# Kernel tuning notes

Hardware: AMD Instinct MI355X
Metric: run time of the kernel (lower is better)

## Reference

```python
import jax, jax.numpy as jnp
import numpy as np


def setup_inputs() -> dict:
    key = jax.random.key(0)
    k1, k2, k3 = jax.random.split(key, 3)
    B, C, H, W = 64, 512, 28, 28
    K = 32
    std = 1.0 / (K * C) ** 0.5
    x = jax.random.normal(k1, (B, C, H, W), dtype=jnp.float32)
    codewords = jax.random.uniform(k2, (K, C), dtype=jnp.float32, minval=-std, maxval=std)
    scale = jax.random.uniform(k3, (K,), dtype=jnp.float32, minval=-1.0, maxval=0.0)
    return {"x": x, "codewords": codewords, "scale": scale}


def reference(x, codewords, scale):
    # x: (B, C, H, W) -> descriptors (B, N, C)
    B, C, H, W = x.shape
    K = codewords.shape[0]
    xd = x.reshape(B, C, H * W).transpose(0, 2, 1)  # (B, N, C)

    # scaled L2: scale_k * ||x_n - c_k||^2, expanded without (B,N,K,C) intermediate
    x_sq = jnp.sum(xd * xd, axis=-1, keepdims=True)            # (B, N, 1)
    c_sq = jnp.sum(codewords * codewords, axis=-1)             # (K,)
    xc = jnp.einsum("bnc,kc->bnk", xd, codewords)              # (B, N, K)
    dist = scale * (x_sq - 2.0 * xc + c_sq)                    # (B, N, K)

    A = jax.nn.softmax(dist, axis=2)                           # (B, N, K)

    # encoded_k = sum_n A[b,n,k] * (x[b,n] - c[k])
    wx = jnp.einsum("bnk,bnc->bkc", A, xd)                     # (B, K, C)
    wsum = jnp.sum(A, axis=1)                                  # (B, K)
    encoded = wx - wsum[:, :, None] * codewords[None, :, :]    # (B, K, C)
    return encoded
```

## Files before the change

### kernel.cpp

```cpp
#include <hip/hip_runtime.h>
#include <hip/hip_bf16.h>

#define BB 64
#define CC 512
#define NPIX 784
#define KK 32
#define NSPL 13
#define PXB 64
#define CW_S 520
#define XS2_S 72

typedef __attribute__((ext_vector_type(8))) short short8;
typedef __attribute__((ext_vector_type(4))) float floatx4;
typedef __attribute__((ext_vector_type(4))) unsigned short ushort4v;

#define OFF_WP 0
#define OFF_WS (NSPL*BB*KK*CC)

__device__ __forceinline__ unsigned short f2bf(float f) {
    union { float f; unsigned u; } v; v.f = f;
    return (unsigned short)((v.u + 0x7FFFu + ((v.u >> 16) & 1u)) >> 16);
}
__device__ __forceinline__ float bf2f(unsigned short h) {
    union { unsigned u; float f; } v; v.u = ((unsigned)h) << 16; return v.f;
}

__global__ __launch_bounds__(256) void k_fused(const float* __restrict__ x,
                                               const float* __restrict__ cw,
                                               const float* __restrict__ scale,
                                               float* __restrict__ ws)
{
    __shared__ __align__(16) unsigned char u8[KK * CW_S * 2];
    __shared__ __align__(16) unsigned short A_l[KK * XS2_S];
    __shared__ float csq_p[8][KK];
    __shared__ float csq_l[KK];
    __shared__ float wred[KK][8];

    unsigned short* cs = (unsigned short*)u8;
    unsigned short* xs = (unsigned short*)u8;

    const int t     = threadIdx.x;
    const int lane  = t & 63;
    const int w     = t >> 6;
    const int col   = lane & 15;
    const int quad  = lane >> 4;
    const int split = blockIdx.x;
    const int b     = blockIdx.y;
    const int p0    = split * PXB;

#pragma unroll 4
    for (int j = 0; j < 16; ++j) {
        const int qidx = t + j * 256;
        const int row = qidx >> 7, qc = qidx & 127;
        const float4 v = *(const float4*)&cw[row * CC + qc * 4];
        ushort4v p; p.x = f2bf(v.x); p.y = f2bf(v.y); p.z = f2bf(v.z); p.w = f2bf(v.w);
        *(ushort4v*)&cs[row * CW_S + qc * 4] = p;
    }
    __syncthreads();
    {
        const int k = t & 31, part = t >> 5;
        float s = 0.f;
        for (int i = 0; i < 64; ++i) {
            const float v = bf2f(cs[k * CW_S + part * 64 + i]);
            s += v * v;
        }
        csq_p[part][k] = s;
    }
    __syncthreads();
    if (t < KK) {
        float s = 0.f;
#pragma unroll
        for (int p = 0; p < 8; ++p) s += csq_p[p][t];
        csq_l[t] = s;
    }
    __syncthreads();

    const float s0 = scale[col], s1 = scale[col + 16];
    const float q0 = csq_l[col], q1 = csq_l[col + 16];

    {
        const int pxg = p0 + w * 16 + col;
        const int px = (pxg < NPIX) ? pxg : (NPIX - 1);
        const float* xb = x + (size_t)b * CC * NPIX + px;

        floatx4 acc0 = {0.f, 0.f, 0.f, 0.f};
        floatx4 acc1 = {0.f, 0.f, 0.f, 0.f};
        float xsqp = 0.f;
        float va[8], vb[8];

#pragma unroll
        for (int j = 0; j < 8; ++j) va[j] = xb[(size_t)(quad * 8 + j) * NPIX];

#pragma unroll
        for (int kc = 0; kc < 16; kc += 2) {
            {
                const int cb = (kc + 1) * 32 + quad * 8;
#pragma unroll
                for (int j = 0; j < 8; ++j) vb[j] = xb[(size_t)(cb + j) * NPIX];
            }
            {
#pragma unroll
                for (int j = 0; j < 8; ++j) xsqp += va[j] * va[j];
                short8 a;
#pragma unroll
                for (int j = 0; j < 8; ++j) a[j] = (short)f2bf(va[j]);
                const int cb0 = kc * 32 + quad * 8;
                const short8 b0 = *(const short8*)&cs[col * CW_S + cb0];
                const short8 b1 = *(const short8*)&cs[(col + 16) * CW_S + cb0];
                acc0 = __builtin_amdgcn_mfma_f32_16x16x32_bf16(a, b0, acc0, 0, 0, 0);
                acc1 = __builtin_amdgcn_mfma_f32_16x16x32_bf16(a, b1, acc1, 0, 0, 0);
            }
            if (kc + 2 < 16) {
                const int cb = (kc + 2) * 32 + quad * 8;
#pragma unroll
                for (int j = 0; j < 8; ++j) va[j] = xb[(size_t)(cb + j) * NPIX];
            }
            {
#pragma unroll
                for (int j = 0; j < 8; ++j) xsqp += vb[j] * vb[j];
                short8 a;
#pragma unroll
                for (int j = 0; j < 8; ++j) a[j] = (short)f2bf(vb[j]);
                const int cb1 = (kc + 1) * 32 + quad * 8;
                const short8 b0 = *(const short8*)&cs[col * CW_S + cb1];
                const short8 b1 = *(const short8*)&cs[(col + 16) * CW_S + cb1];
                acc0 = __builtin_amdgcn_mfma_f32_16x16x32_bf16(a, b0, acc0, 0, 0, 0);
                acc1 = __builtin_amdgcn_mfma_f32_16x16x32_bf16(a, b1, acc1, 0, 0, 0);
            }
        }

        xsqp += __shfl_xor(xsqp, 16);
        xsqp += __shfl_xor(xsqp, 32);

#pragma unroll
        for (int r = 0; r < 4; ++r) {
            const int pl = w * 16 + quad * 4 + r;
            const float xq = __shfl(xsqp, quad * 4 + r);
            const float d0 = s0 * (xq + q0 - 2.f * acc0[r]);
            const float d1 = s1 * (xq + q1 - 2.f * acc1[r]);
            float mx = fmaxf(d0, d1);
            mx = fmaxf(mx, __shfl_xor(mx, 1));
            mx = fmaxf(mx, __shfl_xor(mx, 2));
            mx = fmaxf(mx, __shfl_xor(mx, 4));
            mx = fmaxf(mx, __shfl_xor(mx, 8));
            const float e0 = __expf(d0 - mx), e1 = __expf(d1 - mx);
            float sm = e0 + e1;
            sm += __shfl_xor(sm, 1);
            sm += __shfl_xor(sm, 2);
            sm += __shfl_xor(sm, 4);
            sm += __shfl_xor(sm, 8);
            const float inv = 1.f / sm;
            const bool valid = (p0 + pl) < NPIX;
            A_l[col * XS2_S + pl]        = valid ? f2bf(e0 * inv) : (unsigned short)0;
            A_l[(col + 16) * XS2_S + pl] = valid ? f2bf(e1 * inv) : (unsigned short)0;
        }
    }
    __syncthreads();

    {
        const int k = t >> 3, part = t & 7;
        float s = 0.f;
#pragma unroll
        for (int i = 0; i < 8; ++i) s += bf2f(A_l[k * XS2_S + part * 8 + i]);
        wred[k][part] = s;
    }
    __syncthreads();
    if (t < KK) {
        float s = 0.f;
#pragma unroll
        for (int p = 0; p < 8; ++p) s += wred[t][p];
        ws[OFF_WS + (size_t)(split * BB + b) * KK + t] = s;
    }

    const float* xbase = x + (size_t)b * CC * NPIX + p0;
    float* Wp = ws + OFF_WP;

    for (int cch = 0; cch < 4; ++cch) {
        __syncthreads();
#pragma unroll 2
        for (int j = 0; j < 8; ++j) {
            const int q = t + j * 256;
            const int row = q >> 4, pq = q & 15;
            ushort4v p;
            if (p0 + pq * 4 < NPIX) {
                const float4 v = *(const float4*)&xbase[(size_t)(cch * 128 + row) * NPIX + pq * 4];
                p.x = f2bf(v.x); p.y = f2bf(v.y); p.z = f2bf(v.z); p.w = f2bf(v.w);
            } else { p.x = 0; p.y = 0; p.z = 0; p.w = 0; }
            *(ushort4v*)&xs[row * XS2_S + pq * 4] = p;
        }
        __syncthreads();

        floatx4 a00 = {0.f,0.f,0.f,0.f}, a01 = {0.f,0.f,0.f,0.f};
        floatx4 a10 = {0.f,0.f,0.f,0.f}, a11 = {0.f,0.f,0.f,0.f};
#pragma unroll
        for (int ks = 0; ks < 2; ++ks) {
            const int off = ks * 32 + quad * 8;
            const short8 av0 = *(const short8*)&A_l[col * XS2_S + off];
            const short8 av1 = *(const short8*)&A_l[(col + 16) * XS2_S + off];
            const short8 bv0 = *(const short8*)&xs[(w * 32 + col) * XS2_S + off];
            const short8 bv1 = *(const short8*)&xs[(w * 32 + 16 + col) * XS2_S + off];
            a00 = __builtin_amdgcn_mfma_f32_16x16x32_bf16(av0, bv0, a00, 0, 0, 0);
            a10 = __builtin_amdgcn_mfma_f32_16x16x32_bf16(av1, bv0, a10, 0, 0, 0);
            a01 = __builtin_amdgcn_mfma_f32_16x16x32_bf16(av0, bv1, a01, 0, 0, 0);
            a11 = __builtin_amdgcn_mfma_f32_16x16x32_bf16(av1, bv1, a11, 0, 0, 0);
        }

        const size_t sb = (size_t)(split * BB + b) * KK;
        const int cb = cch * 128 + w * 32;
#pragma unroll
        for (int r = 0; r < 4; ++r) {
            const int k0 = quad * 4 + r;
            Wp[(sb + k0) * CC + cb + col]           = a00[r];
            Wp[(sb + k0) * CC + cb + 16 + col]      = a01[r];
            Wp[(sb + k0 + 16) * CC + cb + col]      = a10[r];
            Wp[(sb + k0 + 16) * CC + cb + 16 + col] = a11[r];
        }
    }
}

__global__ __launch_bounds__(256) void k3(const float* __restrict__ cw,
                                          const float* __restrict__ ws,
                                          float* __restrict__ out)
{
    const int idx = blockIdx.x * 256 + threadIdx.x;
    const int c4 = idx & 127;
    const int k  = (idx >> 7) & 31;
    const int b  = idx >> 12;

    const float* Wp = ws + OFF_WP;
    float4 s = make_float4(0.f, 0.f, 0.f, 0.f);
#pragma unroll
    for (int sp = 0; sp < NSPL; ++sp) {
        const float4 v = *(const float4*)&Wp[((size_t)(sp * BB + b) * KK + k) * CC + c4 * 4];
        s.x += v.x; s.y += v.y; s.z += v.z; s.w += v.w;
    }
    float wsum = 0.f;
#pragma unroll
    for (int sp = 0; sp < NSPL; ++sp) wsum += ws[OFF_WS + (size_t)(sp * BB + b) * KK + k];

    const float4 c4f = *(const float4*)&cw[k * CC + c4 * 4];
    float4 o;
    o.x = s.x - wsum * c4f.x;
    o.y = s.y - wsum * c4f.y;
    o.z = s.z - wsum * c4f.z;
    o.w = s.w - wsum * c4f.w;
    *(float4*)&out[(size_t)idx * 4] = o;
}

extern "C" void kernel_launch(void* const* d_in, const int* in_sizes, int n_in,
                              void* d_out, int out_size, void* d_ws, size_t ws_size,
                              hipStream_t stream) {
    const float* x     = (const float*)d_in[0];
    const float* cw    = (const float*)d_in[1];
    const float* scale = (const float*)d_in[2];
    float* out = (float*)d_out;
    float* ws  = (float*)d_ws;

    k_fused<<<dim3(NSPL, BB), dim3(256), 0, stream>>>(x, cw, scale, ws);
    k3<<<dim3(BB * KK * CC / 4 / 256), dim3(256), 0, stream>>>(cw, ws, out);
}
```

Measured before the change: 192.3 us.

## Precompute bf16 codeword fragments in prep kernel and stage x via async LDS loads

Adds a small prep kernel that converts the codewords once into MFMA-fragment-ordered bf16 and computes the codeword squared norms. Each fused block no longer rebuilds the converted codewords and their norms in shared memory, and reads B fragments directly from global or L2. The first GEMM stage now streams x into double-buffered LDS with global_load_lds, replacing strided per-thread global loads with coalesced 16-byte rows. The cost is an extra kernel launch, B fragments fetched from L2 rather than LDS, and a shared-memory layout that the later stage reuses. Codeword norms are now taken from the fp32 values rather than the bf16-rounded ones, which changes numerics slightly.

```diff
diff --git a/kernel.cpp b/kernel.cpp
--- a/kernel.cpp
+++ b/kernel.cpp
@@ -7,15 +7,17 @@
 #define KK 32
 #define NSPL 13
 #define PXB 64
-#define CW_S 520
+#define NCHK 8
 #define XS2_S 72
 
 typedef __attribute__((ext_vector_type(8))) short short8;
 typedef __attribute__((ext_vector_type(4))) float floatx4;
 typedef __attribute__((ext_vector_type(4))) unsigned short ushort4v;
 
-#define OFF_WP 0
-#define OFF_WS (NSPL*BB*KK*CC)
+#define OFF_BF  0
+#define OFF_CSQ 8192
+#define OFF_WP  8256
+#define OFF_WS2 (OFF_WP + NSPL*BB*KK*CC)
 
 __device__ __forceinline__ unsigned short f2bf(float f) {
     union { float f; unsigned u; } v; v.f = f;
@@ -25,19 +27,51 @@
     union { unsigned u; float f; } v; v.u = ((unsigned)h) << 16; return v.f;
 }
 
+__global__ __launch_bounds__(256) void kprep(const float* __restrict__ cw,
+                                             float* __restrict__ ws)
+{
+    const int t = threadIdx.x;
+    if (blockIdx.x < 8) {
+        const int idx  = blockIdx.x * 256 + t;
+        const int lane = idx & 63;
+        const int pair = idx >> 6;
+        const int row  = (pair & 1) * 16 + (lane & 15);
+        const int cb   = (pair >> 1) * 32 + (lane >> 4) * 8;
+        unsigned short* Bf = (unsigned short*)(ws + OFF_BF);
+        ushort4v pa, pb;
+        pa.x = f2bf(cw[row * CC + cb + 0]); pa.y = f2bf(cw[row * CC + cb + 1]);
+        pa.z = f2bf(cw[row * CC + cb + 2]); pa.w = f2bf(cw[row * CC + cb + 3]);
+        pb.x = f2bf(cw[row * CC + cb + 4]); pb.y = f2bf(cw[row * CC + cb + 5]);
+        pb.z = f2bf(cw[row * CC + cb + 6]); pb.w = f2bf(cw[row * CC + cb + 7]);
+        *(ushort4v*)&Bf[(size_t)idx * 8]     = pa;
+        *(ushort4v*)&Bf[(size_t)idx * 8 + 4] = pb;
+    } else {
+        __shared__ float red[8][KK];
+        const int k = t & 31, part = t >> 5;
+        float s = 0.f;
+#pragma unroll 4
+        for (int i = 0; i < 64; ++i) {
+            const float v = cw[k * CC + part * 64 + i];
+            s += v * v;
+        }
+        red[part][k] = s;
+        __syncthreads();
+        if (t < KK) {
+            float s2 = 0.f;
+#pragma unroll
+            for (int p = 0; p < 8; ++p) s2 += red[p][t];
+            ws[OFF_CSQ + t] = s2;
+        }
+    }
+}
+
 __global__ __launch_bounds__(256) void k_fused(const float* __restrict__ x,
-                                               const float* __restrict__ cw,
                                                const float* __restrict__ scale,
                                                float* __restrict__ ws)
 {
-    __shared__ __align__(16) unsigned char u8[KK * CW_S * 2];
+    __shared__ __align__(16) float xbuf[2][64 * 64];
     __shared__ __align__(16) unsigned short A_l[KK * XS2_S];
-    __shared__ float csq_p[8][KK];
-    __shared__ float csq_l[KK];
     __shared__ float wred[KK][8];
-
-    unsigned short* cs = (unsigned short*)u8;
-    unsigned short* xs = (unsigned short*)u8;
 
     const int t     = threadIdx.x;
     const int lane  = t & 63;
@@ -48,130 +82,96 @@
     const int b     = blockIdx.y;
     const int p0    = split * PXB;
 
-#pragma unroll 4
-    for (int j = 0; j < 16; ++j) {
-        const int qidx = t + j * 256;
-        const int row = qidx >> 7, qc = qidx & 127;
-        const float4 v = *(const float4*)&cw[row * CC + qc * 4];
-        ushort4v p; p.x = f2bf(v.x); p.y = f2bf(v.y); p.z = f2bf(v.z); p.w = f2bf(v.w);
-        *(ushort4v*)&cs[row * CW_S + qc * 4] = p;
+    const unsigned short* Bf = (const unsigned short*)(ws + OFF_BF);
+    const float* xlim = x + (size_t)BB * CC * NPIX - 4;
+
+    auto stage = [&](int ch, int buf) {
+#pragma unroll
+        for (int i = 0; i < 4; ++i) {
+            const int r0 = w * 16 + i * 4;
+            const float* g = x + ((size_t)b * CC + ch * 64 + r0 + (lane >> 4)) * NPIX
+                               + p0 + (lane & 15) * 4;
+            if (g > xlim) g = xlim;
+            __builtin_amdgcn_global_load_lds(
+                (const __attribute__((address_space(1))) void*)g,
+                (__attribute__((address_space(3))) void*)&xbuf[buf][r0 * 64],
+                16, 0, 0);
+        }
+    };
+
+    floatx4 acc0 = {0.f, 0.f, 0.f, 0.f};
+    floatx4 acc1 = {0.f, 0.f, 0.f, 0.f};
+    float xsqp = 0.f;
+
+    stage(0, 0);
+    for (int ch = 0; ch < NCHK; ++ch) {
+        __syncthreads();
+        if (ch + 1 < NCHK) stage(ch + 1, (ch + 1) & 1);
+        const float* xb = xbuf[ch & 1];
+#pragma unroll
+        for (int ks = 0; ks < 2; ++ks) {
+            const int kc = ch * 2 + ks;
+            float v[8];
+#pragma unroll
+            for (int j = 0; j < 8; ++j)
+                v[j] = xb[(ks * 32 + quad * 8 + j) * 64 + w * 16 + col];
+#pragma unroll
+            for (int j = 0; j < 8; ++j) xsqp += v[j] * v[j];
+            short8 a;
+#pragma unroll
+            for (int j = 0; j < 8; ++j) a[j] = (short)f2bf(v[j]);
+            const short8 b0 = *(const short8*)&Bf[(size_t)((kc * 2 + 0) * 64 + lane) * 8];
+            const short8 b1 = *(const short8*)&Bf[(size_t)((kc * 2 + 1) * 64 + lane) * 8];
+            acc0 = __builtin_amdgcn_mfma_f32_16x16x32_bf16(a, b0, acc0, 0, 0, 0);
+            acc1 = __builtin_amdgcn_mfma_f32_16x16x32_bf16(a, b1, acc1, 0, 0, 0);
+        }
+    }
+
+    xsqp += __shfl_xor(xsqp, 16);
+    xsqp += __shfl_xor(xsqp, 32);
+
+    const float s0 = scale[col], s1 = scale[col + 16];
+    const float q0 = ws[OFF_CSQ + col], q1 = ws[OFF_CSQ + col + 16];
+#pragma unroll
+    for (int r = 0; r < 4; ++r) {
+        const int pl = w * 16 + quad * 4 + r;
+        const float xq = __shfl(xsqp, quad * 4 + r);
+        const float d0 = s0 * (xq + q0 - 2.f * acc0[r]);
+        const float d1 = s1 * (xq + q1 - 2.f * acc1[r]);
+        float mx = fmaxf(d0, d1);
+        mx = fmaxf(mx, __shfl_xor(mx, 1));
+        mx = fmaxf(mx, __shfl_xor(mx, 2));
+        mx = fmaxf(mx, __shfl_xor(mx, 4));
+        mx = fmaxf(mx, __shfl_xor(mx, 8));
+        const float e0 = __expf(d0 - mx), e1 = __expf(d1 - mx);
+        float sm = e0 + e1;
+        sm += __shfl_xor(sm, 1);
+        sm += __shfl_xor(sm, 2);
+        sm += __shfl_xor(sm, 4);
+        sm += __shfl_xor(sm, 8);
+        const float inv = 1.f / sm;
+        const bool valid = (p0 + pl) < NPIX;
+        A_l[col * XS2_S + pl]        = valid ? f2bf(e0 * inv) : (unsigned short)0;
+        A_l[(col + 16) * XS2_S + pl] = valid ? f2bf(e1 * inv) : (unsigned short)0;
     }
     __syncthreads();
+
     {
-        const int k = t & 31, part = t >> 5;
+        const int k = t >> 3, part = t & 7;
         float s = 0.f;
-        for (int i = 0; i < 64; ++i) {
-            const float v = bf2f(cs[k * CW_S + part * 64 + i]);
-            s += v * v;
-        }
-        csq_p[part][k] = s;
+#pragma unroll
+        for (int i = 0; i < 8; ++i) s += bf2f(A_l[k * XS2_S + part * 8 + i]);
+        wred[k][part] = s;
     }
     __syncthreads();
     if (t < KK) {
         float s = 0.f;
 #pragma unroll
-        for (int p = 0; p < 8; ++p) s += csq_p[p][t];
-        csq_l[t] = s;
-    }
-    __syncthreads();
-
-    const float s0 = scale[col], s1 = scale[col + 16];
-    const float q0 = csq_l[col], q1 = csq_l[col + 16];
-
-    {
-        const int pxg = p0 + w * 16 + col;
-        const int px = (pxg < NPIX) ? pxg : (NPIX - 1);
-        const float* xb = x + (size_t)b * CC * NPIX + px;
-
-        floatx4 acc0 = {0.f, 0.f, 0.f, 0.f};
-        floatx4 acc1 = {0.f, 0.f, 0.f, 0.f};
-        float xsqp = 0.f;
-        float va[8], vb[8];
-
-#pragma unroll
-        for (int j = 0; j < 8; ++j) va[j] = xb[(size_t)(quad * 8 + j) * NPIX];
-
-#pragma unroll
-        for (int kc = 0; kc < 16; kc += 2) {
-            {
-                const int cb = (kc + 1) * 32 + quad * 8;
-#pragma unroll
-                for (int j = 0; j < 8; ++j) vb[j] = xb[(size_t)(cb + j) * NPIX];
-            }
-            {
-#pragma unroll
-                for (int j = 0; j < 8; ++j) xsqp += va[j] * va[j];
-                short8 a;
-#pragma unroll
-                for (int j = 0; j < 8; ++j) a[j] = (short)f2bf(va[j]);
-                const int cb0 = kc * 32 + quad * 8;
-                const short8 b0 = *(const short8*)&cs[col * CW_S + cb0];
-                const short8 b1 = *(const short8*)&cs[(col + 16) * CW_S + cb0];
-                acc0 = __builtin_amdgcn_mfma_f32_16x16x32_bf16(a, b0, acc0, 0, 0, 0);
-                acc1 = __builtin_amdgcn_mfma_f32_16x16x32_bf16(a, b1, acc1, 0, 0, 0);
-            }
-            if (kc + 2 < 16) {
-                const int cb = (kc + 2) * 32 + quad * 8;
-#pragma unroll
-                for (int j = 0; j < 8; ++j) va[j] = xb[(size_t)(cb + j) * NPIX];
-            }
-            {
-#pragma unroll
-                for (int j = 0; j < 8; ++j) xsqp += vb[j] * vb[j];
-                short8 a;
-#pragma unroll
-                for (int j = 0; j < 8; ++j) a[j] = (short)f2bf(vb[j]);
-                const int cb1 = (kc + 1) * 32 + quad * 8;
-                const short8 b0 = *(const short8*)&cs[col * CW_S + cb1];
-                const short8 b1 = *(const short8*)&cs[(col + 16) * CW_S + cb1];
-                acc0 = __builtin_amdgcn_mfma_f32_16x16x32_bf16(a, b0, acc0, 0, 0, 0);
-                acc1 = __builtin_amdgcn_mfma_f32_16x16x32_bf16(a, b1, acc1, 0, 0, 0);
-            }
-        }
-
-        xsqp += __shfl_xor(xsqp, 16);
-        xsqp += __shfl_xor(xsqp, 32);
-
-#pragma unroll
-        for (int r = 0; r < 4; ++r) {
-            const int pl = w * 16 + quad * 4 + r;
-            const float xq = __shfl(xsqp, quad * 4 + r);
-            const float d0 = s0 * (xq + q0 - 2.f * acc0[r]);
-            const float d1 = s1 * (xq + q1 - 2.f * acc1[r]);
-            float mx = fmaxf(d0, d1);
-            mx = fmaxf(mx, __shfl_xor(mx, 1));
-            mx = fmaxf(mx, __shfl_xor(mx, 2));
-            mx = fmaxf(mx, __shfl_xor(mx, 4));
-            mx = fmaxf(mx, __shfl_xor(mx, 8));
-            const float e0 = __expf(d0 - mx), e1 = __expf(d1 - mx);
-            float sm = e0 + e1;
-            sm += __shfl_xor(sm, 1);
-            sm += __shfl_xor(sm, 2);
-            sm += __shfl_xor(sm, 4);
-            sm += __shfl_xor(sm, 8);
-            const float inv = 1.f / sm;
-            const bool valid = (p0 + pl) < NPIX;
-            A_l[col * XS2_S + pl]        = valid ? f2bf(e0 * inv) : (unsigned short)0;
-            A_l[(col + 16) * XS2_S + pl] = valid ? f2bf(e1 * inv) : (unsigned short)0;
-        }
-    }
-    __syncthreads();
-
-    {
-        const int k = t >> 3, part = t & 7;
-        float s = 0.f;
-#pragma unroll
-        for (int i = 0; i < 8; ++i) s += bf2f(A_l[k * XS2_S + part * 8 + i]);
-        wred[k][part] = s;
-    }
-    __syncthreads();
-    if (t < KK) {
-        float s = 0.f;
-#pragma unroll
         for (int p = 0; p < 8; ++p) s += wred[t][p];
-        ws[OFF_WS + (size_t)(split * BB + b) * KK + t] = s;
-    }
-
+        ws[OFF_WS2 + (size_t)(split * BB + b) * KK + t] = s;
+    }
+
+    unsigned short* xs = (unsigned short*)&xbuf[0][0];
     const float* xbase = x + (size_t)b * CC * NPIX + p0;
     float* Wp = ws + OFF_WP;
 
@@ -236,7 +236,7 @@
     }
     float wsum = 0.f;
 #pragma unroll
-    for (int sp = 0; sp < NSPL; ++sp) wsum += ws[OFF_WS + (size_t)(sp * BB + b) * KK + k];
+    for (int sp = 0; sp < NSPL; ++sp) wsum += ws[OFF_WS2 + (size_t)(sp * BB + b) * KK + k];
 
     const float4 c4f = *(const float4*)&cw[k * CC + c4 * 4];
     float4 o;
@@ -256,6 +256,7 @@
     float* out = (float*)d_out;
     float* ws  = (float*)d_ws;
 
-    k_fused<<<dim3(NSPL, BB), dim3(256), 0, stream>>>(x, cw, scale, ws);
+    kprep<<<dim3(9), dim3(256), 0, stream>>>(cw, ws);
+    k_fused<<<dim3(NSPL, BB), dim3(256), 0, stream>>>(x, scale, ws);
     k3<<<dim3(BB * KK * CC / 4 / 256), dim3(256), 0, stream>>>(cw, ws, out);
 }
```

New measurement: 192.8 us. About the same (+0.3%).
